# Optimization experiments

Hardware: AMD Instinct MI355X
Metric: run time of the kernel (lower is better)

## Reference

```python
import jax, jax.numpy as jnp
import numpy as np

WH, WW = 8, 8
NUM_HEADS = 8
DIM = 256
MLP_HIDDEN = 1024
EPS = 1e-5


def _rel_pos_index(wh, ww):
    ch, cw = np.meshgrid(np.arange(wh), np.arange(ww), indexing='ij')
    flat = np.stack([ch.ravel(), cw.ravel()])            # (2, N)
    rel = flat[:, :, None] - flat[:, None, :]            # (2, N, N)
    rel = rel.transpose(1, 2, 0).copy()                  # (N, N, 2)
    rel[:, :, 0] += wh - 1
    rel[:, :, 1] += ww - 1
    rel[:, :, 0] *= 2 * ww - 1
    return jnp.asarray(rel.sum(-1))                      # (N, N) int

REL_IDX = _rel_pos_index(WH, WW)


def _layernorm(x, g, b):
    mu = x.mean(-1, keepdims=True)
    var = ((x - mu) ** 2).mean(-1, keepdims=True)
    return (x - mu) * jax.lax.rsqrt(var + EPS) * g + b


def _window_partition(x):
    B, H, W, C = x.shape
    x = x.reshape(B, H // WH, WH, W // WW, WW, C)
    return x.transpose(0, 1, 3, 2, 4, 5).reshape(-1, WH * WW, C)


def _window_reverse(w, B, H, W):
    C = w.shape[-1]
    x = w.reshape(B, H // WH, W // WW, WH, WW, C)
    return x.transpose(0, 1, 3, 2, 4, 5).reshape(B, H, W, C)


def _window_attn(qx, kvx, qw, qb, kvw, kvb, bias_table, pw, pb):
    # qx/kvx: [Bw, N, C]; weights stored as [in, out] (torch Linear transposed)
    Bw, N, C = qx.shape
    hd = C // NUM_HEADS
    scale = hd ** -0.5
    q = (qx @ qw + qb).reshape(Bw, N, NUM_HEADS, hd).transpose(0, 2, 1, 3) * scale
    kv = (kvx @ kvw + kvb).reshape(Bw, N, 2, NUM_HEADS, hd)
    k = kv[:, :, 0].transpose(0, 2, 1, 3)
    v = kv[:, :, 1].transpose(0, 2, 1, 3)
    attn = jnp.einsum('bhnd,bhmd->bhnm', q, k)
    bias = bias_table[REL_IDX.reshape(-1)].reshape(N, N, NUM_HEADS).transpose(2, 0, 1)
    attn = jax.nn.softmax(attn + bias[None], axis=-1)
    out = jnp.einsum('bhnm,bhmd->bhnd', attn, v).transpose(0, 2, 1, 3).reshape(Bw, N, C)
    return out @ pw + pb


def setup_inputs() -> dict:
    key = jax.random.key(0)
    ks = jax.random.split(key, 16)
    B, H, W, C = 4, 160, 160, DIM
    nW = (H // WH) * (W // WW)
    N = WH * WW
    n_bias = (2 * WH - 1) * (2 * WW - 1)  # 225
    s = 0.02
    return {
        'x': jax.random.normal(ks[0], (B, H, W, C), jnp.float32),
        'enc_feat': jax.random.normal(ks[1], (B, H, W, C), jnp.float32),
        'mask_matrix': jnp.zeros((nW, N, N), jnp.float32),
        'norm1_g': jnp.ones((C,), jnp.float32),
        'norm1_b': jnp.zeros((C,), jnp.float32),
        'q1_w': jax.random.normal(ks[2], (C, C), jnp.float32) * s,
        'q1_b': jnp.zeros((C,), jnp.float32),
        'kv1_w': jax.random.normal(ks[3], (C, 2 * C), jnp.float32) * s,
        'kv1_b': jnp.zeros((2 * C,), jnp.float32),
        'bias1': jax.random.normal(ks[4], (n_bias, NUM_HEADS), jnp.float32) * s,
        'proj1_w': jax.random.normal(ks[5], (C, C), jnp.float32) * s,
        'proj1_b': jnp.zeros((C,), jnp.float32),
        'q2_w': jax.random.normal(ks[6], (C, C), jnp.float32) * s,
        'q2_b': jnp.zeros((C,), jnp.float32),
        'kv2_w': jax.random.normal(ks[7], (C, 2 * C), jnp.float32) * s,
        'kv2_b': jnp.zeros((2 * C,), jnp.float32),
        'bias2': jax.random.normal(ks[8], (n_bias, NUM_HEADS), jnp.float32) * s,
        'proj2_w': jax.random.normal(ks[9], (C, C), jnp.float32) * s,
        'proj2_b': jnp.zeros((C,), jnp.float32),
        'norm2_g': jnp.ones((C,), jnp.float32),
        'norm2_b': jnp.zeros((C,), jnp.float32),
        'fc1_w': jax.random.normal(ks[10], (C, MLP_HIDDEN), jnp.float32) * s,
        'fc1_b': jnp.zeros((MLP_HIDDEN,), jnp.float32),
        'fc2_w': jax.random.normal(ks[11], (MLP_HIDDEN, C), jnp.float32) * s,
        'fc2_b': jnp.zeros((C,), jnp.float32),
    }


def reference(x, enc_feat, mask_matrix, norm1_g, norm1_b, q1_w, q1_b, kv1_w, kv1_b,
              bias1, proj1_w, proj1_b, q2_w, q2_b, kv2_w, kv2_b, bias2, proj2_w,
              proj2_b, norm2_g, norm2_b, fc1_w, fc1_b, fc2_w, fc2_b):
    # NOTE: the source forward never passes mask_matrix into attention; faithful here.
    B, H, W, C = x.shape
    shortcut = x
    xn = _layernorm(x, norm1_g, norm1_b)
    xw = _window_partition(xn)              # [B*nW, N, C]
    ew = _window_partition(enc_feat)        # [B*nW, N, C]
    # windowed self-attention with relative position bias
    xw = _window_attn(xw, xw, q1_w, q1_b, kv1_w, kv1_b, bias1, proj1_w, proj1_b)
    # windowed cross-attention to encoder features
    xw = _window_attn(xw, ew, q2_w, q2_b, kv2_w, kv2_b, bias2, proj2_w, proj2_b)
    x = shortcut + _window_reverse(xw, B, H, W)
    h = _layernorm(x, norm2_g, norm2_b)
    h = jax.nn.gelu(h @ fc1_w + fc1_b, approximate=False) @ fc2_w + fc2_b
    return x + h
```

## Files before the change

kernel.cpp:

```cpp
#include <hip/hip_runtime.h>

typedef __attribute__((ext_vector_type(4))) float f32x4;
typedef __attribute__((ext_vector_type(8))) short bf16x8;
typedef __attribute__((ext_vector_type(8))) unsigned short ushort8;
typedef unsigned short u16;
typedef unsigned int u32;

__device__ __forceinline__ u16 f2b(float f) {
    u32 u = __builtin_bit_cast(u32, f);
    u32 r = (u + 0x7fffu + ((u >> 16) & 1u)) >> 16;
    return (u16)r;
}

struct PrepAll {
    const float* src[8];
    u16* dst[8];
    int K[8];
    int N[8];
    float S[8];
};

__global__ __launch_bounds__(256) void prep_w(PrepAll p) {
    const int wi = blockIdx.y;
    const int K = p.K[wi], N = p.N[wi];
    const int e = blockIdx.x * 256 + threadIdx.x;
    if (e >= K * N) return;
    const int k = e / N, n = e % N;
    p.dst[wi][n * K + k] = f2b(p.src[wi][e] * p.S[wi]);
}

__global__ __launch_bounds__(64) void prep_bias(const float* __restrict__ t1,
                                                const float* __restrict__ t2,
                                                float* __restrict__ Bm) {
    const int j = threadIdx.x;
    const int i = blockIdx.x;
    const int hh = blockIdx.y;
    const int s = hh >> 3, h = hh & 7;
    const int idx = ((i >> 3) - (j >> 3) + 7) * 15 + ((i & 7) - (j & 7) + 7);
    const float* tab = s ? t2 : t1;
    Bm[(long)hh * 4096 + i * 64 + j] = tab[idx * 8 + h];
}

__global__ __launch_bounds__(256) void prep_bcat(const float* __restrict__ q1b,
                                                 const float* __restrict__ kv1b,
                                                 const float* __restrict__ q2b,
                                                 float qs, float* __restrict__ b1cat,
                                                 float* __restrict__ q2bs) {
    const int g = blockIdx.x * 256 + threadIdx.x;
    if (g < 256) {
        b1cat[g] = qs * q1b[g];
        q2bs[g] = qs * q2b[g];
    } else if (g < 768) {
        b1cat[g] = kv1b[g - 256];
    }
}

__global__ __launch_bounds__(256) void cast_bf(const float* __restrict__ in,
                                               u16* __restrict__ out) {
    const long i = (long)blockIdx.x * 256 + threadIdx.x;
    const float4 a = *(const float4*)(in + i * 8);
    const float4 b = *(const float4*)(in + i * 8 + 4);
    ushort8 o;
    o[0] = f2b(a.x); o[1] = f2b(a.y); o[2] = f2b(a.z); o[3] = f2b(a.w);
    o[4] = f2b(b.x); o[5] = f2b(b.y); o[6] = f2b(b.z); o[7] = f2b(b.w);
    *(ushort8*)(out + i * 8) = o;
}

__global__ __launch_bounds__(256) void ln256(const float* __restrict__ x,
                                             const float* __restrict__ g,
                                             const float* __restrict__ b,
                                             u16* __restrict__ out) {
    const int lane = threadIdx.x & 63;
    const long row = (long)blockIdx.x * 4 + (threadIdx.x >> 6);
    const float4 v = *(const float4*)(x + row * 256 + lane * 4);
    float s = v.x + v.y + v.z + v.w;
    float s2 = v.x * v.x + v.y * v.y + v.z * v.z + v.w * v.w;
#pragma unroll
    for (int off = 32; off > 0; off >>= 1) {
        s += __shfl_xor(s, off);
        s2 += __shfl_xor(s2, off);
    }
    const float mu = s * (1.f / 256.f);
    const float var = s2 * (1.f / 256.f) - mu * mu;
    const float rr = rsqrtf(var + 1e-5f);
    const int c = lane * 4;
    const float4 gv = *(const float4*)(g + c);
    const float4 bv = *(const float4*)(b + c);
    ushort4 o;
    o.x = f2b((v.x - mu) * rr * gv.x + bv.x);
    o.y = f2b((v.y - mu) * rr * gv.y + bv.y);
    o.z = f2b((v.z - mu) * rr * gv.z + bv.z);
    o.w = f2b((v.w - mu) * rr * gv.w + bv.w);
    *(ushort4*)(out + row * 256 + c) = o;
}

#define LSTR 40

template <int EPI, int NT>
__global__ __launch_bounds__(256, 3) void gemmP(const u16* __restrict__ A,
                                                const u16* __restrict__ Bt,
                                                const float* __restrict__ bias,
                                                const float* __restrict__ res,
                                                u16* outb, float* outf,
                                                int N, int Nt) {
    constexpr int K = NT * 32;
    __shared__ u16 ldsA[2][128 * LSTR];
    __shared__ u16 ldsB[2][128 * LSTR];
    const int t = threadIdx.x;
    const int lane = t & 63;
    const int wave = t >> 6;
    const int wr = wave >> 1, wc = wave & 1;
    const int l15 = lane & 15, lg = lane >> 4;

    const int per = gridDim.x >> 3;
    const int id2 = (blockIdx.x & 7) * per + (blockIdx.x >> 3);
    const int bm = id2 / Nt, bn = id2 % Nt;
    const long m0 = (long)bm * 128;
    const int n0 = bn * 128;

    const int srow = t >> 2, skc = (t & 3) * 8;
    const u16* Ag = A + (m0 + srow) * K + skc;
    const u16* Bg = Bt + (long)(n0 + srow) * K + skc;

    bf16x8 ra[3][2], rb[3][2];

#define LOAD_TILE(s, kt)                                            \
    do {                                                            \
        ra[s][0] = *(const bf16x8*)(Ag + (kt) * 32);                \
        ra[s][1] = *(const bf16x8*)(Ag + (long)64 * K + (kt) * 32); \
        rb[s][0] = *(const bf16x8*)(Bg + (kt) * 32);                \
        rb[s][1] = *(const bf16x8*)(Bg + (long)64 * K + (kt) * 32); \
    } while (0)

#define WRITE_TILE(s, buf)                                              \
    do {                                                                \
        *(bf16x8*)&ldsA[buf][srow * LSTR + skc] = ra[s][0];             \
        *(bf16x8*)&ldsA[buf][(srow + 64) * LSTR + skc] = ra[s][1];      \
        *(bf16x8*)&ldsB[buf][srow * LSTR + skc] = rb[s][0];             \
        *(bf16x8*)&ldsB[buf][(srow + 64) * LSTR + skc] = rb[s][1];      \
    } while (0)

    f32x4 acc[4][4];
#pragma unroll
    for (int i = 0; i < 4; i++)
#pragma unroll
        for (int j = 0; j < 4; j++) acc[i][j] = (f32x4){0.f, 0.f, 0.f, 0.f};

    LOAD_TILE(0, 0);
    if (NT > 1) LOAD_TILE(1, 1);
    if (NT > 2) LOAD_TILE(2, 2);
    WRITE_TILE(0, 0);
    asm volatile("s_waitcnt lgkmcnt(0)" ::: "memory");
    __builtin_amdgcn_s_barrier();
    __builtin_amdgcn_sched_barrier(0);

#pragma unroll
    for (int tt = 0; tt < NT; ++tt) {
        const int cur = tt & 1;
        bf16x8 af[4], bfr[4];
#pragma unroll
        for (int i = 0; i < 4; i++)
            af[i] = *(const bf16x8*)&ldsA[cur][(wr * 64 + i * 16 + l15) * LSTR + lg * 8];
#pragma unroll
        for (int i = 0; i < 4; i++)
            bfr[i] = *(const bf16x8*)&ldsB[cur][(wc * 64 + i * 16 + l15) * LSTR + lg * 8];

        if (tt + 3 < NT) LOAD_TILE(tt % 3, tt + 3);
        if (tt + 1 < NT) WRITE_TILE((tt + 1) % 3, 1 - cur);

#pragma unroll
        for (int mi = 0; mi < 4; mi++)
#pragma unroll
            for (int ni = 0; ni < 4; ni++)
                acc[mi][ni] = __builtin_amdgcn_mfma_f32_16x16x32_bf16(af[mi], bfr[ni], acc[mi][ni], 0, 0, 0);

        if (tt + 1 < NT) {
            asm volatile("s_waitcnt lgkmcnt(0)" ::: "memory");
            __builtin_amdgcn_s_barrier();
            __builtin_amdgcn_sched_barrier(0);
        }
    }
#undef LOAD_TILE
#undef WRITE_TILE

#pragma unroll
    for (int mi = 0; mi < 4; mi++) {
#pragma unroll
        for (int ni = 0; ni < 4; ni++) {
            const int col = n0 + wc * 64 + ni * 16 + l15;
            const float bv = bias[col];
#pragma unroll
            for (int r = 0; r < 4; r++) {
                const long row = m0 + wr * 64 + mi * 16 + lg * 4 + r;
                float v = acc[mi][ni][r] + bv;
                if (EPI == 2) v = 0.5f * v * (1.f + erff(v * 0.70710678118f));
                const long idx = row * N + col;
                if (EPI == 3)
                    outf[idx] = v + res[idx];
                else
                    outb[idx] = f2b(v);
            }
        }
    }
}

__global__ __launch_bounds__(256) void attn64(const u16* __restrict__ Q, int qs,
                                              const u16* __restrict__ KV, int ks,
                                              const float* __restrict__ Bm,
                                              u16* __restrict__ AO) {
    __shared__ u16 Plds[4][64 * 72];
    __shared__ u16 Vt[4][32 * 72];
    const int lane = threadIdx.x & 63, wave = threadIdx.x >> 6;
    const int wh = blockIdx.x * 4 + wave;
    const int w = wh >> 3, h = wh & 7;
    const int b = w / 400, rem = w % 400;
    const int wy = rem / 20, wx = rem % 20;
    const long base_t = (long)b * 25600 + wy * 8 * 160 + wx * 8;
    const int l15 = lane & 15, lg = lane >> 4;

    bf16x8 qf[4], kf[4];
#pragma unroll
    for (int ti = 0; ti < 4; ti++) {
        const int r = ti * 16 + l15;
        const long tt = base_t + (r >> 3) * 160 + (r & 7);
        qf[ti] = *(const bf16x8*)(Q + tt * qs + h * 32 + lg * 8);
        kf[ti] = *(const bf16x8*)(KV + tt * ks + h * 32 + lg * 8);
    }
    const f32x4 zz = (f32x4){0.f, 0.f, 0.f, 0.f};
    f32x4 s[4][4];
#pragma unroll
    for (int ti = 0; ti < 4; ti++)
#pragma unroll
        for (int tj = 0; tj < 4; tj++)
            s[ti][tj] = __builtin_amdgcn_mfma_f32_16x16x32_bf16(qf[ti], kf[tj], zz, 0, 0, 0);

    {
        const long tt = base_t + (lane >> 3) * 160 + (lane & 7);
        const u16* vrow = KV + tt * ks + 256 + h * 32;
#pragma unroll
        for (int cg = 0; cg < 4; cg++) {
            bf16x8 v8 = *(const bf16x8*)(vrow + cg * 8);
#pragma unroll
            for (int j = 0; j < 8; j++) Vt[wave][(cg * 8 + j) * 72 + lane] = (u16)v8[j];
        }
    }

    const float* Bh = Bm + h * 4096;
#pragma unroll
    for (int ti = 0; ti < 4; ti++) {
#pragma unroll
        for (int r = 0; r < 4; r++) {
            const int i = ti * 16 + lg * 4 + r;
            float vv[4];
            float m = -1e30f;
#pragma unroll
            for (int tj = 0; tj < 4; tj++) {
                vv[tj] = s[ti][tj][r] + Bh[i * 64 + tj * 16 + l15];
                m = fmaxf(m, vv[tj]);
            }
#pragma unroll
            for (int off = 1; off < 16; off <<= 1) m = fmaxf(m, __shfl_xor(m, off));
            float sum = 0.f;
#pragma unroll
            for (int tj = 0; tj < 4; tj++) {
                vv[tj] = __expf(vv[tj] - m);
                sum += vv[tj];
            }
#pragma unroll
            for (int off = 1; off < 16; off <<= 1) sum += __shfl_xor(sum, off);
            const float inv = 1.f / sum;
#pragma unroll
            for (int tj = 0; tj < 4; tj++)
                Plds[wave][i * 72 + tj * 16 + l15] = f2b(vv[tj] * inv);
        }
    }

    f32x4 o[4][2];
#pragma unroll
    for (int mi = 0; mi < 4; mi++)
#pragma unroll
        for (int n = 0; n < 2; n++) o[mi][n] = zz;
#pragma unroll
    for (int c = 0; c < 2; c++) {
        bf16x8 vf[2];
#pragma unroll
        for (int n = 0; n < 2; n++)
            vf[n] = *(const bf16x8*)(&Vt[wave][(n * 16 + l15) * 72 + c * 32 + lg * 8]);
#pragma unroll
        for (int mi = 0; mi < 4; mi++) {
            bf16x8 pf = *(const bf16x8*)(&Plds[wave][(mi * 16 + l15) * 72 + c * 32 + lg * 8]);
#pragma unroll
            for (int n = 0; n < 2; n++)
                o[mi][n] = __builtin_amdgcn_mfma_f32_16x16x32_bf16(pf, vf[n], o[mi][n], 0, 0, 0);
        }
    }
#pragma unroll
    for (int mi = 0; mi < 4; mi++) {
#pragma unroll
        for (int n = 0; n < 2; n++) {
#pragma unroll
            for (int r = 0; r < 4; r++) {
                const int i = mi * 16 + lg * 4 + r;
                const long tt = base_t + (i >> 3) * 160 + (i & 7);
                AO[tt * 256 + h * 32 + n * 16 + l15] = f2b(o[mi][n][r]);
            }
        }
    }
}

extern "C" void kernel_launch(void* const* d_in, const int* in_sizes, int n_in,
                              void* d_out, int out_size, void* d_ws, size_t ws_size,
                              hipStream_t stream) {
    const float* x    = (const float*)d_in[0];
    const float* enc  = (const float*)d_in[1];
    const float* n1g  = (const float*)d_in[3];
    const float* n1b  = (const float*)d_in[4];
    const float* q1w  = (const float*)d_in[5];
    const float* q1b  = (const float*)d_in[6];
    const float* kv1w = (const float*)d_in[7];
    const float* kv1b = (const float*)d_in[8];
    const float* bias1 = (const float*)d_in[9];
    const float* p1w  = (const float*)d_in[10];
    const float* p1b  = (const float*)d_in[11];
    const float* q2w  = (const float*)d_in[12];
    const float* q2b  = (const float*)d_in[13];
    const float* kv2w = (const float*)d_in[14];
    const float* kv2b = (const float*)d_in[15];
    const float* bias2 = (const float*)d_in[16];
    const float* p2w  = (const float*)d_in[17];
    const float* p2b  = (const float*)d_in[18];
    const float* n2g  = (const float*)d_in[19];
    const float* n2b  = (const float*)d_in[20];
    const float* f1w  = (const float*)d_in[21];
    const float* f1b  = (const float*)d_in[22];
    const float* f2w  = (const float*)d_in[23];
    const float* f2bias = (const float*)d_in[24];
    float* out = (float*)d_out;

    char* ws = (char*)d_ws;
    size_t off = 0;
    auto alloc = [&](size_t bytes) {
        char* p = ws + off;
        off += (bytes + 255) & ~(size_t)255;
        return p;
    };
    u16* Wt    = (u16*)alloc(1048576 * 2);
    float* Bm  = (float*)alloc(16 * 4096 * 4);
    float* b1c = (float*)alloc(768 * 4);
    float* q2s = (float*)alloc(256 * 4);
    u16* xn    = (u16*)alloc(52428800);
    u16* qb    = (u16*)alloc(52428800);
    u16* kvb   = (u16*)alloc(104857600);
    u16* ao    = (u16*)alloc(52428800);
    u16* encb  = (u16*)alloc(52428800);

    u16* qkv = qb;
    u16* h1  = kvb;

    u16 *q1t = Wt, *p1t = Wt + 196608, *q2t = Wt + 262144,
        *kv2t = Wt + 327680, *p2t = Wt + 458752, *f1t = Wt + 524288, *f2t = Wt + 786432;

    const float qscale = 0.17677669529663687f;

    PrepAll pa;
    pa.src[0] = q1w;  pa.dst[0] = q1t;        pa.K[0] = 256;  pa.N[0] = 256;  pa.S[0] = qscale;
    pa.src[1] = kv1w; pa.dst[1] = Wt + 65536; pa.K[1] = 256;  pa.N[1] = 512;  pa.S[1] = 1.f;
    pa.src[2] = p1w;  pa.dst[2] = p1t;        pa.K[2] = 256;  pa.N[2] = 256;  pa.S[2] = 1.f;
    pa.src[3] = q2w;  pa.dst[3] = q2t;        pa.K[3] = 256;  pa.N[3] = 256;  pa.S[3] = qscale;
    pa.src[4] = kv2w; pa.dst[4] = kv2t;       pa.K[4] = 256;  pa.N[4] = 512;  pa.S[4] = 1.f;
    pa.src[5] = p2w;  pa.dst[5] = p2t;        pa.K[5] = 256;  pa.N[5] = 256;  pa.S[5] = 1.f;
    pa.src[6] = f1w;  pa.dst[6] = f1t;        pa.K[6] = 256;  pa.N[6] = 1024; pa.S[6] = 1.f;
    pa.src[7] = f2w;  pa.dst[7] = f2t;        pa.K[7] = 1024; pa.N[7] = 256;  pa.S[7] = 1.f;
    prep_w<<<dim3(1024, 8), 256, 0, stream>>>(pa);
    prep_bias<<<dim3(64, 16), 64, 0, stream>>>(bias1, bias2, Bm);
    prep_bcat<<<dim3(3), 256, 0, stream>>>(q1b, kv1b, q2b, qscale, b1c, q2s);
    cast_bf<<<dim3(12800), 256, 0, stream>>>(enc, encb);
    ln256<<<dim3(25600), 256, 0, stream>>>(x, n1g, n1b, xn);

    gemmP<0, 8><<<dim3(4800), 256, 0, stream>>>(xn, q1t, b1c, nullptr, qkv, nullptr, 768, 6);
    attn64<<<dim3(3200), 256, 0, stream>>>(qkv, 768, qkv + 256, 768, Bm, ao);
    gemmP<0, 8><<<dim3(1600), 256, 0, stream>>>(ao, p1t, p1b, nullptr, xn, nullptr, 256, 2);

    gemmP<0, 8><<<dim3(1600), 256, 0, stream>>>(xn, q2t, q2s, nullptr, qb, nullptr, 256, 2);
    gemmP<0, 8><<<dim3(3200), 256, 0, stream>>>(encb, kv2t, kv2b, nullptr, kvb, nullptr, 512, 4);
    attn64<<<dim3(3200), 256, 0, stream>>>(qb, 256, kvb, 512, Bm + 8 * 4096, ao);

    gemmP<3, 8><<<dim3(1600), 256, 0, stream>>>(ao, p2t, p2b, x, (u16*)nullptr, out, 256, 2);

    ln256<<<dim3(25600), 256, 0, stream>>>(out, n2g, n2b, qb);
    for (int c = 0; c < 2; c++) {
        const u16* xh = qb + (size_t)c * 51200 * 256;
        float* oc = out + (size_t)c * 51200 * 256;
        gemmP<2, 8><<<dim3(3200), 256, 0, stream>>>(xh, f1t, f1b, nullptr, h1, nullptr, 1024, 8);
        gemmP<3, 32><<<dim3(800), 256, 0, stream>>>(h1, f2t, f2bias, oc, (u16*)nullptr, oc, 256, 2);
    }
}
```

Before: 794.3 us.

## Rewrite GEMM with per-wave register A streaming and LDS-staged coalesced epilogue

Replaces the 128x128 double-buffered LDS GEMM with a 256x64 tile in which each wave streams its own 64 rows of A straight from global memory into registers, triple-buffered. Only the B tile (64 x 256 K-chunk) goes through LDS, loaded once per 256-wide K chunk. The epilogue now stages results through LDS so that each lane writes whole contiguous rows with vector stores, and the fp32 residual path reads the residual with vector loads. This is meant to cut LDS traffic and barriers and to coalesce output writes, at the cost of uncoalesced per-lane A global loads and fewer N-tiles per block.

```diff
diff --git a/kernel.cpp b/kernel.cpp
--- a/kernel.cpp
+++ b/kernel.cpp
@@ -94,51 +94,30 @@
     *(ushort4*)(out + row * 256 + c) = o;
 }
 
-#define LSTR 40
-
-template <int EPI, int NT>
-__global__ __launch_bounds__(256, 3) void gemmP(const u16* __restrict__ A,
+template <int EPI, int KTILES>
+__global__ __launch_bounds__(256, 3) void wgemm(const u16* __restrict__ A,
                                                 const u16* __restrict__ Bt,
                                                 const float* __restrict__ bias,
                                                 const float* __restrict__ res,
-                                                u16* outb, float* outf,
+                                                u16* __restrict__ outb,
+                                                float* __restrict__ outf,
                                                 int N, int Nt) {
-    constexpr int K = NT * 32;
-    __shared__ u16 ldsA[2][128 * LSTR];
-    __shared__ u16 ldsB[2][128 * LSTR];
-    const int t = threadIdx.x;
-    const int lane = t & 63;
-    const int wave = t >> 6;
-    const int wr = wave >> 1, wc = wave & 1;
+    constexpr int K = KTILES * 256;
+    constexpr int STEPS = KTILES * 8;
+    __shared__ u16 LDSU[18432];
+
+    const int t = threadIdx.x, lane = t & 63, wave = t >> 6;
     const int l15 = lane & 15, lg = lane >> 4;
 
     const int per = gridDim.x >> 3;
     const int id2 = (blockIdx.x & 7) * per + (blockIdx.x >> 3);
     const int bm = id2 / Nt, bn = id2 % Nt;
-    const long m0 = (long)bm * 128;
-    const int n0 = bn * 128;
-
-    const int srow = t >> 2, skc = (t & 3) * 8;
-    const u16* Ag = A + (m0 + srow) * K + skc;
-    const u16* Bg = Bt + (long)(n0 + srow) * K + skc;
-
-    bf16x8 ra[3][2], rb[3][2];
-
-#define LOAD_TILE(s, kt)                                            \
-    do {                                                            \
-        ra[s][0] = *(const bf16x8*)(Ag + (kt) * 32);                \
-        ra[s][1] = *(const bf16x8*)(Ag + (long)64 * K + (kt) * 32); \
-        rb[s][0] = *(const bf16x8*)(Bg + (kt) * 32);                \
-        rb[s][1] = *(const bf16x8*)(Bg + (long)64 * K + (kt) * 32); \
-    } while (0)
-
-#define WRITE_TILE(s, buf)                                              \
-    do {                                                                \
-        *(bf16x8*)&ldsA[buf][srow * LSTR + skc] = ra[s][0];             \
-        *(bf16x8*)&ldsA[buf][(srow + 64) * LSTR + skc] = ra[s][1];      \
-        *(bf16x8*)&ldsB[buf][srow * LSTR + skc] = rb[s][0];             \
-        *(bf16x8*)&ldsB[buf][(srow + 64) * LSTR + skc] = rb[s][1];      \
-    } while (0)
+    const long m0 = (long)bm * 256;
+    const int n0 = bn * 64;
+
+    const u16* Aw = A + (m0 + wave * 64 + l15) * K + lg * 8;
+    const int brow = t >> 2;
+    const u16* Bg = Bt + (long)(n0 + brow) * K + (t & 3) * 64;
 
     f32x4 acc[4][4];
 #pragma unroll
@@ -146,60 +125,105 @@
 #pragma unroll
         for (int j = 0; j < 4; j++) acc[i][j] = (f32x4){0.f, 0.f, 0.f, 0.f};
 
-    LOAD_TILE(0, 0);
-    if (NT > 1) LOAD_TILE(1, 1);
-    if (NT > 2) LOAD_TILE(2, 2);
-    WRITE_TILE(0, 0);
-    asm volatile("s_waitcnt lgkmcnt(0)" ::: "memory");
+    bf16x8 af[3][4];
+    auto lda = [&](int set, int s) {
+#pragma unroll
+        for (int mi = 0; mi < 4; mi++)
+            af[set][mi] = *(const bf16x8*)(Aw + (long)mi * 16 * K + s * 32);
+    };
+
+    auto loadB = [&](int kc, bool first) {
+        if (!first) __builtin_amdgcn_s_barrier();
+        bf16x8 tmp[4];
+#pragma unroll
+        for (int half = 0; half < 2; half++) {
+#pragma unroll
+            for (int j = 0; j < 4; j++)
+                tmp[j] = *(const bf16x8*)(Bg + kc * 256 + half * 32 + j * 8);
+#pragma unroll
+            for (int j = 0; j < 4; j++)
+                *(bf16x8*)&LDSU[brow * 264 + (t & 3) * 64 + half * 32 + j * 8] = tmp[j];
+        }
+        asm volatile("s_waitcnt lgkmcnt(0)" ::: "memory");
+        __builtin_amdgcn_sched_barrier(0);
+        __builtin_amdgcn_s_barrier();
+    };
+
+    lda(0, 0);
+    lda(1, 1);
+    lda(2, 2);
+
+#pragma unroll
+    for (int s = 0; s < STEPS; ++s) {
+        if ((s & 7) == 0) loadB(s >> 3, s == 0);
+        bf16x8 bfr[4];
+#pragma unroll
+        for (int ni = 0; ni < 4; ni++)
+            bfr[ni] = *(const bf16x8*)&LDSU[(ni * 16 + l15) * 264 + (s & 7) * 32 + lg * 8];
+#pragma unroll
+        for (int mi = 0; mi < 4; mi++)
+#pragma unroll
+            for (int ni = 0; ni < 4; ni++)
+                acc[mi][ni] = __builtin_amdgcn_mfma_f32_16x16x32_bf16(af[s % 3][mi], bfr[ni], acc[mi][ni], 0, 0, 0);
+        if (s + 3 < STEPS) lda(s % 3, s + 3);
+    }
+
     __builtin_amdgcn_s_barrier();
-    __builtin_amdgcn_sched_barrier(0);
-
-#pragma unroll
-    for (int tt = 0; tt < NT; ++tt) {
-        const int cur = tt & 1;
-        bf16x8 af[4], bfr[4];
-#pragma unroll
-        for (int i = 0; i < 4; i++)
-            af[i] = *(const bf16x8*)&ldsA[cur][(wr * 64 + i * 16 + l15) * LSTR + lg * 8];
-#pragma unroll
-        for (int i = 0; i < 4; i++)
-            bfr[i] = *(const bf16x8*)&ldsB[cur][(wc * 64 + i * 16 + l15) * LSTR + lg * 8];
-
-        if (tt + 3 < NT) LOAD_TILE(tt % 3, tt + 3);
-        if (tt + 1 < NT) WRITE_TILE((tt + 1) % 3, 1 - cur);
-
-#pragma unroll
-        for (int mi = 0; mi < 4; mi++)
-#pragma unroll
-            for (int ni = 0; ni < 4; ni++)
-                acc[mi][ni] = __builtin_amdgcn_mfma_f32_16x16x32_bf16(af[mi], bfr[ni], acc[mi][ni], 0, 0, 0);
-
-        if (tt + 1 < NT) {
+    const long rowbase = m0 + wave * 64 + lane;
+
+    if (EPI == 3) {
+        float* EF = (float*)&LDSU[wave * 4608];
+#pragma unroll
+        for (int p = 0; p < 2; p++) {
+#pragma unroll
+            for (int mi = 0; mi < 4; mi++) {
+#pragma unroll
+                for (int nh = 0; nh < 2; nh++) {
+                    const int ni = p * 2 + nh;
+                    const float bv = bias[n0 + ni * 16 + l15];
+#pragma unroll
+                    for (int r = 0; r < 4; r++)
+                        EF[(mi * 16 + lg * 4 + r) * 36 + nh * 16 + l15] = acc[mi][ni][r] + bv;
+                }
+            }
             asm volatile("s_waitcnt lgkmcnt(0)" ::: "memory");
-            __builtin_amdgcn_s_barrier();
             __builtin_amdgcn_sched_barrier(0);
-        }
-    }
-#undef LOAD_TILE
-#undef WRITE_TILE
-
-#pragma unroll
-    for (int mi = 0; mi < 4; mi++) {
-#pragma unroll
-        for (int ni = 0; ni < 4; ni++) {
-            const int col = n0 + wc * 64 + ni * 16 + l15;
-            const float bv = bias[col];
-#pragma unroll
-            for (int r = 0; r < 4; r++) {
-                const long row = m0 + wr * 64 + mi * 16 + lg * 4 + r;
-                float v = acc[mi][ni][r] + bv;
-                if (EPI == 2) v = 0.5f * v * (1.f + erff(v * 0.70710678118f));
-                const long idx = row * N + col;
-                if (EPI == 3)
-                    outf[idx] = v + res[idx];
-                else
-                    outb[idx] = f2b(v);
-            }
+#pragma unroll
+            for (int j = 0; j < 8; j++) {
+                f32x4 cv = *(f32x4*)&EF[lane * 36 + j * 4];
+                const long idx = rowbase * N + n0 + p * 32 + j * 4;
+                const float4 rv = *(const float4*)(res + idx);
+                f32x4 ov;
+                ov[0] = cv[0] + rv.x; ov[1] = cv[1] + rv.y;
+                ov[2] = cv[2] + rv.z; ov[3] = cv[3] + rv.w;
+                *(f32x4*)(outf + idx) = ov;
+            }
+            if (p == 0) {
+                asm volatile("s_waitcnt lgkmcnt(0)" ::: "memory");
+                __builtin_amdgcn_sched_barrier(0);
+            }
+        }
+    } else {
+        u16* E = &LDSU[wave * 4608];
+#pragma unroll
+        for (int mi = 0; mi < 4; mi++) {
+#pragma unroll
+            for (int ni = 0; ni < 4; ni++) {
+                const float bv = bias[n0 + ni * 16 + l15];
+#pragma unroll
+                for (int r = 0; r < 4; r++) {
+                    float v = acc[mi][ni][r] + bv;
+                    if (EPI == 2) v = 0.5f * v * (1.f + erff(v * 0.70710678118f));
+                    E[(mi * 16 + lg * 4 + r) * 72 + ni * 16 + l15] = f2b(v);
+                }
+            }
+        }
+        asm volatile("s_waitcnt lgkmcnt(0)" ::: "memory");
+        __builtin_amdgcn_sched_barrier(0);
+#pragma unroll
+        for (int j = 0; j < 8; j++) {
+            bf16x8 cv = *(bf16x8*)&E[lane * 72 + j * 8];
+            *(bf16x8*)(outb + rowbase * N + n0 + j * 8) = cv;
         }
     }
 }
@@ -377,21 +401,21 @@
     cast_bf<<<dim3(12800), 256, 0, stream>>>(enc, encb);
     ln256<<<dim3(25600), 256, 0, stream>>>(x, n1g, n1b, xn);
 
-    gemmP<0, 8><<<dim3(4800), 256, 0, stream>>>(xn, q1t, b1c, nullptr, qkv, nullptr, 768, 6);
+    wgemm<0, 1><<<dim3(4800), 256, 0, stream>>>(xn, q1t, b1c, nullptr, qkv, nullptr, 768, 12);
     attn64<<<dim3(3200), 256, 0, stream>>>(qkv, 768, qkv + 256, 768, Bm, ao);
-    gemmP<0, 8><<<dim3(1600), 256, 0, stream>>>(ao, p1t, p1b, nullptr, xn, nullptr, 256, 2);
-
-    gemmP<0, 8><<<dim3(1600), 256, 0, stream>>>(xn, q2t, q2s, nullptr, qb, nullptr, 256, 2);
-    gemmP<0, 8><<<dim3(3200), 256, 0, stream>>>(encb, kv2t, kv2b, nullptr, kvb, nullptr, 512, 4);
+    wgemm<0, 1><<<dim3(1600), 256, 0, stream>>>(ao, p1t, p1b, nullptr, xn, nullptr, 256, 4);
+
+    wgemm<0, 1><<<dim3(1600), 256, 0, stream>>>(xn, q2t, q2s, nullptr, qb, nullptr, 256, 4);
+    wgemm<0, 1><<<dim3(3200), 256, 0, stream>>>(encb, kv2t, kv2b, nullptr, kvb, nullptr, 512, 8);
     attn64<<<dim3(3200), 256, 0, stream>>>(qb, 256, kvb, 512, Bm + 8 * 4096, ao);
 
-    gemmP<3, 8><<<dim3(1600), 256, 0, stream>>>(ao, p2t, p2b, x, (u16*)nullptr, out, 256, 2);
+    wgemm<3, 1><<<dim3(1600), 256, 0, stream>>>(ao, p2t, p2b, x, nullptr, out, 256, 4);
 
     ln256<<<dim3(25600), 256, 0, stream>>>(out, n2g, n2b, qb);
     for (int c = 0; c < 2; c++) {
         const u16* xh = qb + (size_t)c * 51200 * 256;
         float* oc = out + (size_t)c * 51200 * 256;
-        gemmP<2, 8><<<dim3(3200), 256, 0, stream>>>(xh, f1t, f1b, nullptr, h1, nullptr, 1024, 8);
-        gemmP<3, 32><<<dim3(800), 256, 0, stream>>>(h1, f2t, f2bias, oc, (u16*)nullptr, oc, 256, 2);
-    }
-}
+        wgemm<2, 1><<<dim3(3200), 256, 0, stream>>>(xh, f1t, f1b, nullptr, h1, nullptr, 1024, 16);
+        wgemm<3, 4><<<dim3(800), 256, 0, stream>>>(h1, f2t, f2bias, oc, nullptr, oc, 256, 4);
+    }
+}
```

After: 1.070 ms. 34.7% more time.

## Replace tiled GEMM with A-stationary row-panel GEMM streaming B from global

Applied to the files above, without the earlier changes.

The 128x128 double-buffered LDS GEMM is replaced by a kernel where each block stages a 64-row by 256-K slice of A in LDS once. It then sweeps all output column groups, streaming B fragments straight from global/L2 into registers with two-deep prefetching. The epilogue runs per 256-column group. A is read from HBM only once and most per-k-step barriers go away, at the cost of B being reloaded by every block and no LDS reuse of B across waves. The fc2 path (K=1024) restages A every 256 K with barriers.

```diff
diff --git a/kernel.cpp b/kernel.cpp
--- a/kernel.cpp
+++ b/kernel.cpp
@@ -94,51 +94,38 @@
     *(ushort4*)(out + row * 256 + c) = o;
 }
 
-#define LSTR 40
-
-template <int EPI, int NT>
-__global__ __launch_bounds__(256, 3) void gemmP(const u16* __restrict__ A,
+template <int EPI, int KT, int NG>
+__global__ __launch_bounds__(256, 3) void sgemm(const u16* __restrict__ A,
                                                 const u16* __restrict__ Bt,
                                                 const float* __restrict__ bias,
                                                 const float* __restrict__ res,
-                                                u16* outb, float* outf,
-                                                int N, int Nt) {
-    constexpr int K = NT * 32;
-    __shared__ u16 ldsA[2][128 * LSTR];
-    __shared__ u16 ldsB[2][128 * LSTR];
-    const int t = threadIdx.x;
-    const int lane = t & 63;
-    const int wave = t >> 6;
-    const int wr = wave >> 1, wc = wave & 1;
+                                                u16* __restrict__ outb,
+                                                float* __restrict__ outf,
+                                                int N) {
+    constexpr int K = KT * 256;
+    constexpr int STEPS = KT * NG * 8;
+    __shared__ u16 As[64 * 264];
+    const int t = threadIdx.x, lane = t & 63, wave = t >> 6;
     const int l15 = lane & 15, lg = lane >> 4;
-
-    const int per = gridDim.x >> 3;
-    const int id2 = (blockIdx.x & 7) * per + (blockIdx.x >> 3);
-    const int bm = id2 / Nt, bn = id2 % Nt;
-    const long m0 = (long)bm * 128;
-    const int n0 = bn * 128;
-
-    const int srow = t >> 2, skc = (t & 3) * 8;
-    const u16* Ag = A + (m0 + srow) * K + skc;
-    const u16* Bg = Bt + (long)(n0 + srow) * K + skc;
-
-    bf16x8 ra[3][2], rb[3][2];
-
-#define LOAD_TILE(s, kt)                                            \
-    do {                                                            \
-        ra[s][0] = *(const bf16x8*)(Ag + (kt) * 32);                \
-        ra[s][1] = *(const bf16x8*)(Ag + (long)64 * K + (kt) * 32); \
-        rb[s][0] = *(const bf16x8*)(Bg + (kt) * 32);                \
-        rb[s][1] = *(const bf16x8*)(Bg + (long)64 * K + (kt) * 32); \
-    } while (0)
-
-#define WRITE_TILE(s, buf)                                              \
-    do {                                                                \
-        *(bf16x8*)&ldsA[buf][srow * LSTR + skc] = ra[s][0];             \
-        *(bf16x8*)&ldsA[buf][(srow + 64) * LSTR + skc] = ra[s][1];      \
-        *(bf16x8*)&ldsB[buf][srow * LSTR + skc] = rb[s][0];             \
-        *(bf16x8*)&ldsB[buf][(srow + 64) * LSTR + skc] = rb[s][1];      \
-    } while (0)
+    const long m0 = (long)blockIdx.x * 64;
+
+    auto stageA = [&](int kc) {
+        const u16* src = A + (m0 + (t >> 2)) * K + kc * 256 + (t & 3) * 64;
+        u16* dst = &As[(t >> 2) * 264 + (t & 3) * 64];
+#pragma unroll
+        for (int j = 0; j < 8; j++)
+            *(bf16x8*)(dst + j * 8) = *(const bf16x8*)(src + j * 8);
+    };
+
+    bf16x8 bset[2][4];
+    auto loadB = [&](int s, int buf) {
+        const int cb = (KT == 1) ? (s >> 3) * 256 : 0;
+        const int ko = (KT == 1) ? (s & 7) * 32 : s * 32;
+        const u16* bp = Bt + (long)(cb + wave * 64 + l15) * K + ko + lg * 8;
+#pragma unroll
+        for (int ni = 0; ni < 4; ni++)
+            bset[buf][ni] = *(const bf16x8*)(bp + (long)ni * 16 * K);
+    };
 
     f32x4 acc[4][4];
 #pragma unroll
@@ -146,62 +133,58 @@
 #pragma unroll
         for (int j = 0; j < 4; j++) acc[i][j] = (f32x4){0.f, 0.f, 0.f, 0.f};
 
-    LOAD_TILE(0, 0);
-    if (NT > 1) LOAD_TILE(1, 1);
-    if (NT > 2) LOAD_TILE(2, 2);
-    WRITE_TILE(0, 0);
+    auto epi = [&](int ng) {
+        const int colb = ng * 256 + wave * 64;
+#pragma unroll
+        for (int mi = 0; mi < 4; mi++) {
+#pragma unroll
+            for (int ni = 0; ni < 4; ni++) {
+                const int col = colb + ni * 16 + l15;
+                const float bv = bias[col];
+#pragma unroll
+                for (int r = 0; r < 4; r++) {
+                    const long row = m0 + mi * 16 + lg * 4 + r;
+                    float v = acc[mi][ni][r] + bv;
+                    if (EPI == 2) v = 0.5f * v * (1.f + erff(v * 0.70710678118f));
+                    const long idx = row * N + col;
+                    if (EPI == 3)
+                        outf[idx] = v + res[idx];
+                    else
+                        outb[idx] = f2b(v);
+                    acc[mi][ni][r] = 0.f;
+                }
+            }
+        }
+    };
+
+    stageA(0);
+    loadB(0, 0);
+    if (STEPS > 1) loadB(1, 1);
     asm volatile("s_waitcnt lgkmcnt(0)" ::: "memory");
     __builtin_amdgcn_s_barrier();
-    __builtin_amdgcn_sched_barrier(0);
-
-#pragma unroll
-    for (int tt = 0; tt < NT; ++tt) {
-        const int cur = tt & 1;
-        bf16x8 af[4], bfr[4];
-#pragma unroll
-        for (int i = 0; i < 4; i++)
-            af[i] = *(const bf16x8*)&ldsA[cur][(wr * 64 + i * 16 + l15) * LSTR + lg * 8];
-#pragma unroll
-        for (int i = 0; i < 4; i++)
-            bfr[i] = *(const bf16x8*)&ldsB[cur][(wc * 64 + i * 16 + l15) * LSTR + lg * 8];
-
-        if (tt + 3 < NT) LOAD_TILE(tt % 3, tt + 3);
-        if (tt + 1 < NT) WRITE_TILE((tt + 1) % 3, 1 - cur);
-
+
+#pragma unroll
+    for (int s = 0; s < STEPS; ++s) {
+        if (KT > 1 && s > 0 && (s & 7) == 0) {
+            __builtin_amdgcn_s_barrier();
+            stageA(s >> 3);
+            asm volatile("s_waitcnt lgkmcnt(0)" ::: "memory");
+            __builtin_amdgcn_sched_barrier(0);
+            __builtin_amdgcn_s_barrier();
+        }
+        bf16x8 af[4];
 #pragma unroll
         for (int mi = 0; mi < 4; mi++)
+            af[mi] = *(const bf16x8*)&As[(mi * 16 + l15) * 264 + (s & 7) * 32 + lg * 8];
+#pragma unroll
+        for (int mi = 0; mi < 4; mi++)
 #pragma unroll
             for (int ni = 0; ni < 4; ni++)
-                acc[mi][ni] = __builtin_amdgcn_mfma_f32_16x16x32_bf16(af[mi], bfr[ni], acc[mi][ni], 0, 0, 0);
-
-        if (tt + 1 < NT) {
-            asm volatile("s_waitcnt lgkmcnt(0)" ::: "memory");
-            __builtin_amdgcn_s_barrier();
-            __builtin_amdgcn_sched_barrier(0);
-        }
-    }
-#undef LOAD_TILE
-#undef WRITE_TILE
-
-#pragma unroll
-    for (int mi = 0; mi < 4; mi++) {
-#pragma unroll
-        for (int ni = 0; ni < 4; ni++) {
-            const int col = n0 + wc * 64 + ni * 16 + l15;
-            const float bv = bias[col];
-#pragma unroll
-            for (int r = 0; r < 4; r++) {
-                const long row = m0 + wr * 64 + mi * 16 + lg * 4 + r;
-                float v = acc[mi][ni][r] + bv;
-                if (EPI == 2) v = 0.5f * v * (1.f + erff(v * 0.70710678118f));
-                const long idx = row * N + col;
-                if (EPI == 3)
-                    outf[idx] = v + res[idx];
-                else
-                    outb[idx] = f2b(v);
-            }
-        }
-    }
+                acc[mi][ni] = __builtin_amdgcn_mfma_f32_16x16x32_bf16(af[mi], bset[s & 1][ni], acc[mi][ni], 0, 0, 0);
+        if (s + 2 < STEPS) loadB(s + 2, s & 1);
+        if (KT == 1 && (s & 7) == 7) epi(s >> 3);
+    }
+    if (KT > 1) epi(0);
 }
 
 __global__ __launch_bounds__(256) void attn64(const u16* __restrict__ Q, int qs,
@@ -377,21 +360,21 @@
     cast_bf<<<dim3(12800), 256, 0, stream>>>(enc, encb);
     ln256<<<dim3(25600), 256, 0, stream>>>(x, n1g, n1b, xn);
 
-    gemmP<0, 8><<<dim3(4800), 256, 0, stream>>>(xn, q1t, b1c, nullptr, qkv, nullptr, 768, 6);
+    sgemm<0, 1, 3><<<dim3(1600), 256, 0, stream>>>(xn, q1t, b1c, nullptr, qkv, nullptr, 768);
     attn64<<<dim3(3200), 256, 0, stream>>>(qkv, 768, qkv + 256, 768, Bm, ao);
-    gemmP<0, 8><<<dim3(1600), 256, 0, stream>>>(ao, p1t, p1b, nullptr, xn, nullptr, 256, 2);
-
-    gemmP<0, 8><<<dim3(1600), 256, 0, stream>>>(xn, q2t, q2s, nullptr, qb, nullptr, 256, 2);
-    gemmP<0, 8><<<dim3(3200), 256, 0, stream>>>(encb, kv2t, kv2b, nullptr, kvb, nullptr, 512, 4);
+    sgemm<0, 1, 1><<<dim3(1600), 256, 0, stream>>>(ao, p1t, p1b, nullptr, xn, nullptr, 256);
+
+    sgemm<0, 1, 1><<<dim3(1600), 256, 0, stream>>>(xn, q2t, q2s, nullptr, qb, nullptr, 256);
+    sgemm<0, 1, 2><<<dim3(1600), 256, 0, stream>>>(encb, kv2t, kv2b, nullptr, kvb, nullptr, 512);
     attn64<<<dim3(3200), 256, 0, stream>>>(qb, 256, kvb, 512, Bm + 8 * 4096, ao);
 
-    gemmP<3, 8><<<dim3(1600), 256, 0, stream>>>(ao, p2t, p2b, x, (u16*)nullptr, out, 256, 2);
+    sgemm<3, 1, 1><<<dim3(1600), 256, 0, stream>>>(ao, p2t, p2b, x, nullptr, out, 256);
 
     ln256<<<dim3(25600), 256, 0, stream>>>(out, n2g, n2b, qb);
     for (int c = 0; c < 2; c++) {
         const u16* xh = qb + (size_t)c * 51200 * 256;
         float* oc = out + (size_t)c * 51200 * 256;
-        gemmP<2, 8><<<dim3(3200), 256, 0, stream>>>(xh, f1t, f1b, nullptr, h1, nullptr, 1024, 8);
-        gemmP<3, 32><<<dim3(800), 256, 0, stream>>>(h1, f2t, f2bias, oc, (u16*)nullptr, oc, 256, 2);
-    }
-}
+        sgemm<2, 1, 4><<<dim3(800), 256, 0, stream>>>(xh, f1t, f1b, nullptr, h1, nullptr, 1024);
+        sgemm<3, 4, 1><<<dim3(800), 256, 0, stream>>>(h1, f2t, f2bias, oc, nullptr, oc, 256);
+    }
+}
```

After: 1.455 ms. +83.1%, slower.
